# Performance work log

Measured on AMD Instinct MI355X. Metric: run time of the kernel, lower is better.

The kernel has to match this reference:

```python
import jax, jax.numpy as jnp
import numpy as np

B, C, N, K = 8, 192, 3136, 9
COUT = 384


def setup_inputs() -> dict:
    key = jax.random.key(0)
    k1, k2, k3, k4 = jax.random.split(key, 4)
    x = jax.random.normal(k1, (B, C, N, 1), dtype=jnp.float32)
    edge_index = jax.random.randint(k2, (2, B, N, K), 0, N, dtype=jnp.int64)
    # 1x1 conv params: BasicConv([2C, COUT]) with bias, act='relu'
    W = jax.random.normal(k3, (COUT, 2 * C), dtype=jnp.float32) * (1.0 / np.sqrt(2 * C))
    b = jax.random.normal(k4, (COUT,), dtype=jnp.float32) * 0.01
    return {"x": x, "edge_index": edge_index, "W": W, "b": b}


def _gather(xs, idx):
    # xs: [B, C, N]; idx: [B, N, K] -> [B, C, N, K]
    return jax.vmap(lambda xb, ib: xb[:, ib])(xs, idx)


def reference(x, edge_index, W, b):
    xs = x[..., 0]                       # [B, C, N]
    x_i = _gather(xs, edge_index[1])     # [B, C, N, K] center features
    x_j = _gather(xs, edge_index[0])     # [B, C, N, K] neighbor features
    feat = jnp.concatenate([x_i, x_j - x_i], axis=1)  # [B, 2C, N, K]
    # 1x1 conv + bias + relu
    h = jnp.einsum('oi,bink->bonk', W, feat) + b[None, :, None, None]
    h = jax.nn.relu(h)                   # [B, COUT, N, K]
    return jnp.max(h, axis=-1, keepdims=True)  # [B, COUT, N, 1]
```

## Files before the change

kernel.cpp:

```cpp
#include <hip/hip_runtime.h>
#include <hip/hip_bf16.h>


#define Bb   8
#define Cc   192
#define Nn   3136
#define Kk   9
#define CO   384
#define TWOC 384
#define JTOT 768
#define PADC 200
#define PADL 256

typedef short  short8 __attribute__((ext_vector_type(8)));
typedef float  f32x4  __attribute__((ext_vector_type(4)));

__device__ __forceinline__ float bf2f(unsigned int u16) {
    union { unsigned int i; float f; } c;
    c.i = u16 << 16;
    return c.f;
}
__device__ __forceinline__ short f2bf(float f) {
    __hip_bfloat16 h = __float2bfloat16(f);
    short s; __builtin_memcpy(&s, &h, 2); return s;
}

__global__ __launch_bounds__(256) void prep_fused(const void* __restrict__ x_,
                                                  const void* __restrict__ W_,
                                                  const int* __restrict__ ei,
                                                  short* __restrict__ xT,
                                                  short* __restrict__ A_Tb,
                                                  int* __restrict__ flags) {
    __shared__ float s[64][33];
    __shared__ int sflag;
    const int tid = threadIdx.x;
    const int bid = blockIdx.x;

    if (tid < 64) {
        unsigned int u = ((const unsigned short*)x_)[2 * tid];
        int bige = (((u >> 7) & 0xFFu) >= 0x88u);
        unsigned long long bf = __ballot(bige);
        int f32 = (bf != 0ull) ? 1 : 0;
        if (tid == 0) sflag = f32;
        if (bid == 0) {
            int oddnz = (ei[2 * tid + 1] != 0);
            unsigned long long bo = __ballot(oddnz);
            if (tid == 0) {
                flags[0] = f32;
                flags[1] = (bo == 0ull) ? 1 : 0;
            }
        }
    }
    __syncthreads();
    const int fp32 = sflag;

    if (bid < 2352) {
        int b   = bid / 294;
        int rem = bid - b * 294;
        int ct  = rem / 49;
        int nt  = rem - ct * 49;
        const int n0 = nt * 64;
        const int c0 = ct * 32;
        const int cl   = tid >> 3;
        const int nseg = tid & 7;

        if (fp32) {
            const float* p = (const float*)x_ + ((size_t)b * Cc + c0 + cl) * Nn + n0 + nseg * 8;
            float4 v0 = *(const float4*)p;
            float4 v1 = *(const float4*)(p + 4);
            int nb = nseg * 8;
            s[nb + 0][cl] = v0.x;  s[nb + 1][cl] = v0.y;
            s[nb + 2][cl] = v0.z;  s[nb + 3][cl] = v0.w;
            s[nb + 4][cl] = v1.x;  s[nb + 5][cl] = v1.y;
            s[nb + 6][cl] = v1.z;  s[nb + 7][cl] = v1.w;
        } else {
            const unsigned short* p = (const unsigned short*)x_ + ((size_t)b * Cc + c0 + cl) * Nn + n0 + nseg * 8;
            ushort4 u0 = *(const ushort4*)p;
            ushort4 u1 = *(const ushort4*)(p + 4);
            int nb = nseg * 8;
            s[nb + 0][cl] = bf2f(u0.x);  s[nb + 1][cl] = bf2f(u0.y);
            s[nb + 2][cl] = bf2f(u0.z);  s[nb + 3][cl] = bf2f(u0.w);
            s[nb + 4][cl] = bf2f(u1.x);  s[nb + 5][cl] = bf2f(u1.y);
            s[nb + 6][cl] = bf2f(u1.z);  s[nb + 7][cl] = bf2f(u1.w);
        }
        __syncthreads();

        const int nl = tid >> 2;
        const int cs = tid & 3;
        short8 o;
#pragma unroll
        for (int i = 0; i < 8; ++i) o[i] = f2bf(s[nl][cs * 8 + i]);
        *(short8*)(xT + ((size_t)b * Nn + n0 + nl) * PADC + c0 + cs * 8) = o;
    } else {
        int t = (bid - 2352) * 256 + tid;
        int j = t / Cc;
        int c = t - j * Cc;
        int row = (j < CO) ? j : (j - CO);
        float w1, w2;
        if (fp32) {
            const float* W = (const float*)W_;
            w1 = W[row * TWOC + c];  w2 = W[row * TWOC + Cc + c];
        } else {
            const unsigned short* W = (const unsigned short*)W_;
            w1 = bf2f(W[row * TWOC + c]);  w2 = bf2f(W[row * TWOC + Cc + c]);
        }
        A_Tb[(size_t)j * PADC + c] = f2bf((j < CO) ? (w1 - w2) : w2);
    }
}

__global__ __launch_bounds__(256) void gemm_mfma(const short* __restrict__ xT,
                                                 const short* __restrict__ A_Tb,
                                                 short* __restrict__ T) {
    __shared__ short Asl[64 * PADL];
    __shared__ short Bsl[64 * PADL];

    const int n0 = blockIdx.x * 64;
    const int j0 = blockIdx.y * 64;
    const int b  = blockIdx.z;
    const int tid  = threadIdx.x;
    const int w    = tid >> 6;
    const int lane = tid & 63;
    const int col  = lane & 15;
    const int quad = lane >> 4;

#pragma unroll
    for (int i = 0; i < 6; ++i) {
        int g    = tid + i * 256;
        int row  = g / 24;
        int slot = g - row * 24;
        int sl   = slot ^ (row & 7);
        *(short8*)(Asl + row * PADL + sl * 8) =
            *(const short8*)(xT + ((size_t)b * Nn + n0 + row) * PADC + slot * 8);
        *(short8*)(Bsl + row * PADL + sl * 8) =
            *(const short8*)(A_Tb + (size_t)(j0 + row) * PADC + slot * 8);
    }
    __syncthreads();

    f32x4 acc[4];
#pragma unroll
    for (int i = 0; i < 4; ++i) acc[i] = (f32x4)(0.0f);

#pragma unroll
    for (int kf = 0; kf < 6; ++kf) {
        const int sl = (kf * 4 + quad) ^ (col & 7);
        short8 bfr = *(const short8*)(Bsl + (w * 16 + col) * PADL + sl * 8);
#pragma unroll
        for (int fm = 0; fm < 4; ++fm) {
            short8 a = *(const short8*)(Asl + (fm * 16 + col) * PADL + sl * 8);
            acc[fm] = __builtin_amdgcn_mfma_f32_16x16x32_bf16(a, bfr, acc[fm], 0, 0, 0);
        }
    }
    __syncthreads();

    short* Ct = Asl;
#pragma unroll
    for (int fm = 0; fm < 4; ++fm) {
#pragma unroll
        for (int r = 0; r < 4; ++r) {
            Ct[(fm * 16 + quad * 4 + r) * 72 + w * 16 + col] = f2bf(acc[fm][r]);
        }
    }
    __syncthreads();

    {
        const int row = tid >> 2;
        const int gq  = tid & 3;
#pragma unroll
        for (int i = 0; i < 2; ++i) {
            int g = gq + i * 4;
            *(short8*)(T + ((size_t)(b * Nn + n0 + row)) * JTOT + j0 + g * 8) =
                *(const short8*)(Ct + row * 72 + g * 8);
        }
    }
}

__global__ __launch_bounds__(384) void gather_max(const int* __restrict__ ei,
                                                  const short* __restrict__ T,
                                                  const void* __restrict__ bias_,
                                                  void* __restrict__ out_,
                                                  const int* __restrict__ flags) {
    __shared__ float sm[32][97];
    __shared__ int si0[32][Kk];
    __shared__ int si1[32][Kk];

    const int fp32 = flags[0];
    const int is64 = flags[1];
    const int bid  = blockIdx.x;
    const int b    = bid & 7;
    const int rest = bid >> 3;
    const int quarter = rest / 98;
    const int n0   = (rest % 98) * 32;
    const int tid  = threadIdx.x;

    for (int s = tid; s < 32 * 2 * Kk; s += 384) {
        int ln = s / (2 * Kk);
        int slot = s - ln * (2 * Kk);
        int n = n0 + ln;
        size_t pos; int* dstp;
        if (slot < Kk) { pos = ((size_t)b * Nn + n) * Kk + slot;               dstp = &si0[ln][slot]; }
        else           { pos = ((size_t)(Bb + b) * Nn + n) * Kk + (slot - Kk); dstp = &si1[ln][slot - Kk]; }
        int v = is64 ? ei[2 * pos] : ei[pos];
        *dstp = (v < 0) ? 0 : (v >= Nn ? Nn - 1 : v);
    }
    __syncthreads();

    const int cg  = tid % 24;
    const int seg = tid / 24;
    const int och = quarter * 96 + cg * 4;
    const unsigned short* Tb = (const unsigned short*)T + (size_t)b * Nn * JTOT;

    float b0, b1, b2, b3;
    if (fp32) {
        const float* bp = (const float*)bias_ + och;
        b0 = bp[0]; b1 = bp[1]; b2 = bp[2]; b3 = bp[3];
    } else {
        const unsigned short* bp = (const unsigned short*)bias_ + och;
        b0 = bf2f(bp[0]); b1 = bf2f(bp[1]); b2 = bf2f(bp[2]); b3 = bf2f(bp[3]);
    }

#pragma unroll
    for (int t = 0; t < 2; ++t) {
        int ln = seg * 2 + t;
        float m0 = -INFINITY, m1 = -INFINITY, m2 = -INFINITY, m3 = -INFINITY;
#pragma unroll
        for (int k = 0; k < Kk; ++k) {
            uint2 uu = *(const uint2*)(Tb + (size_t)si1[ln][k] * JTOT + och);
            uint2 vv = *(const uint2*)(Tb + (size_t)si0[ln][k] * JTOT + CO + och);
            m0 = fmaxf(m0, bf2f(uu.x & 0xffffu) + bf2f(vv.x & 0xffffu));
            m1 = fmaxf(m1, bf2f(uu.x >> 16)     + bf2f(vv.x >> 16));
            m2 = fmaxf(m2, bf2f(uu.y & 0xffffu) + bf2f(vv.y & 0xffffu));
            m3 = fmaxf(m3, bf2f(uu.y >> 16)     + bf2f(vv.y >> 16));
        }
        sm[ln][cg * 4 + 0] = fmaxf(m0 + b0, 0.0f);
        sm[ln][cg * 4 + 1] = fmaxf(m1 + b1, 0.0f);
        sm[ln][cg * 4 + 2] = fmaxf(m2 + b2, 0.0f);
        sm[ln][cg * 4 + 3] = fmaxf(m3 + b3, 0.0f);
    }
    __syncthreads();

    const int g = tid >> 5, l = tid & 31;
    if (fp32) {
        float* op = (float*)out_;
#pragma unroll
        for (int rr = 0; rr < 8; ++rr) {
            int ol = g * 8 + rr;
            int o  = quarter * 96 + ol;
            op[((size_t)b * CO + o) * Nn + n0 + l] = sm[l][ol];
        }
    } else {
        __hip_bfloat16* op = (__hip_bfloat16*)out_;
#pragma unroll
        for (int rr = 0; rr < 8; ++rr) {
            int ol = g * 8 + rr;
            int o  = quarter * 96 + ol;
            op[((size_t)b * CO + o) * Nn + n0 + l] = __float2bfloat16(sm[l][ol]);
        }
    }
}

extern "C" void kernel_launch(void* const* d_in, const int* in_sizes, int n_in,
                              void* d_out, int out_size, void* d_ws, size_t ws_size,
                              hipStream_t stream) {
    const void* x  = d_in[0];
    const int*  ei = (const int*)d_in[1];
    const void* W  = d_in[2];
    const void* bs = d_in[3];

    char* ws = (char*)d_ws;
    int*   flags = (int*)ws;
    short* A_Tb  = (short*)(ws + 1024);
    short* xT    = (short*)(ws + (512u << 10));
    short* T     = (short*)(ws + (11u << 20));

    prep_fused<<<2352 + 576, 256, 0, stream>>>(x, W, ei, xT, A_Tb, flags);

    dim3 g1(Nn / 64, JTOT / 64, Bb);
    gemm_mfma<<<g1, 256, 0, stream>>>(xT, A_Tb, T);

    gather_max<<<Bb * 4 * (Nn / 32), 384, 0, stream>>>(ei, T, bs, d_out, flags);
}
```

Before: 136.7 us.

## Use direct global-to-LDS loads in GEMM and widen gather loads to 16 bytes

The GEMM tile staging now uses global_load_lds 16-byte transfers instead of loading through registers, with the swizzle moved to the global source address. The gather-max kernel gives each thread 8 output channels and one node (instead of 4 channels and two nodes), so each neighbor fetch is a single 16-byte load. It also precomputes byte offsets in shared memory and decodes bf16 with cheaper mask and shift operations. The aim is fewer load instructions and less VGPR traffic. The risks are per-lane LDS placement correctness for the direct loads and lower memory-level parallelism per thread.

```diff
diff --git a/kernel.cpp b/kernel.cpp
--- a/kernel.cpp
+++ b/kernel.cpp
@@ -20,9 +20,24 @@
     c.i = u16 << 16;
     return c.f;
 }
+__device__ __forceinline__ float bflo(unsigned int u) {
+    union { unsigned int i; float f; } c;
+    c.i = u << 16;
+    return c.f;
+}
+__device__ __forceinline__ float bfhi(unsigned int u) {
+    union { unsigned int i; float f; } c;
+    c.i = u & 0xffff0000u;
+    return c.f;
+}
 __device__ __forceinline__ short f2bf(float f) {
     __hip_bfloat16 h = __float2bfloat16(f);
     short s; __builtin_memcpy(&s, &h, 2); return s;
+}
+__device__ __forceinline__ void gload16(const void* g, void* l) {
+    __builtin_amdgcn_global_load_lds(
+        (const __attribute__((address_space(1))) unsigned int*)g,
+        (__attribute__((address_space(3))) unsigned int*)l, 16, 0, 0);
 }
 
 __global__ __launch_bounds__(256) void prep_fused(const void* __restrict__ x_,
@@ -123,16 +138,18 @@
     const int col  = lane & 15;
     const int quad = lane >> 4;
 
-#pragma unroll
-    for (int i = 0; i < 6; ++i) {
-        int g    = tid + i * 256;
-        int row  = g / 24;
-        int slot = g - row * 24;
-        int sl   = slot ^ (row & 7);
-        *(short8*)(Asl + row * PADL + sl * 8) =
-            *(const short8*)(xT + ((size_t)b * Nn + n0 + row) * PADC + slot * 8);
-        *(short8*)(Bsl + row * PADL + sl * 8) =
-            *(const short8*)(A_Tb + (size_t)(j0 + row) * PADC + slot * 8);
+    {
+        const int rh = lane >> 5;
+        const int s  = lane & 31;
+#pragma unroll
+        for (int t = 0; t < 8; ++t) {
+            const int row = w * 16 + t * 2 + rh;
+            const int sw  = s ^ (row & 7);
+            const short* gA = xT   + ((size_t)b * Nn + n0 + row) * PADC + sw * 8;
+            const short* gB = A_Tb + (size_t)(j0 + row) * PADC + sw * 8;
+            gload16(gA, Asl + (w * 16 + t * 2) * PADL);
+            gload16(gB, Bsl + (w * 16 + t * 2) * PADL);
+        }
     }
     __syncthreads();
 
@@ -180,8 +197,8 @@
                                                   void* __restrict__ out_,
                                                   const int* __restrict__ flags) {
     __shared__ float sm[32][97];
-    __shared__ int si0[32][Kk];
-    __shared__ int si1[32][Kk];
+    __shared__ int soff0[32][Kk];
+    __shared__ int soff1[32][Kk];
 
     const int fp32 = flags[0];
     const int is64 = flags[1];
@@ -197,45 +214,57 @@
         int slot = s - ln * (2 * Kk);
         int n = n0 + ln;
         size_t pos; int* dstp;
-        if (slot < Kk) { pos = ((size_t)b * Nn + n) * Kk + slot;               dstp = &si0[ln][slot]; }
-        else           { pos = ((size_t)(Bb + b) * Nn + n) * Kk + (slot - Kk); dstp = &si1[ln][slot - Kk]; }
+        if (slot < Kk) { pos = ((size_t)b * Nn + n) * Kk + slot;               dstp = &soff0[ln][slot]; }
+        else           { pos = ((size_t)(Bb + b) * Nn + n) * Kk + (slot - Kk); dstp = &soff1[ln][slot - Kk]; }
         int v = is64 ? ei[2 * pos] : ei[pos];
-        *dstp = (v < 0) ? 0 : (v >= Nn ? Nn - 1 : v);
-    }
-    __syncthreads();
-
-    const int cg  = tid % 24;
-    const int seg = tid / 24;
-    const int och = quarter * 96 + cg * 4;
-    const unsigned short* Tb = (const unsigned short*)T + (size_t)b * Nn * JTOT;
-
-    float b0, b1, b2, b3;
+        v = (v < 0) ? 0 : (v >= Nn ? Nn - 1 : v);
+        *dstp = v * (JTOT * 2);
+    }
+    __syncthreads();
+
+    const int cg  = tid % 12;
+    const int seg = tid / 12;
+    const int och = quarter * 96 + cg * 8;
+    const char* Tb = (const char*)T + (size_t)b * Nn * JTOT * 2;
+    const char* Tu = Tb + (size_t)och * 2;
+    const char* Tv = Tb + (size_t)(CO + och) * 2;
+
+    float bv[8];
     if (fp32) {
         const float* bp = (const float*)bias_ + och;
-        b0 = bp[0]; b1 = bp[1]; b2 = bp[2]; b3 = bp[3];
+#pragma unroll
+        for (int j = 0; j < 8; ++j) bv[j] = bp[j];
     } else {
         const unsigned short* bp = (const unsigned short*)bias_ + och;
-        b0 = bf2f(bp[0]); b1 = bf2f(bp[1]); b2 = bf2f(bp[2]); b3 = bf2f(bp[3]);
-    }
-
-#pragma unroll
-    for (int t = 0; t < 2; ++t) {
-        int ln = seg * 2 + t;
-        float m0 = -INFINITY, m1 = -INFINITY, m2 = -INFINITY, m3 = -INFINITY;
-#pragma unroll
-        for (int k = 0; k < Kk; ++k) {
-            uint2 uu = *(const uint2*)(Tb + (size_t)si1[ln][k] * JTOT + och);
-            uint2 vv = *(const uint2*)(Tb + (size_t)si0[ln][k] * JTOT + CO + och);
-            m0 = fmaxf(m0, bf2f(uu.x & 0xffffu) + bf2f(vv.x & 0xffffu));
-            m1 = fmaxf(m1, bf2f(uu.x >> 16)     + bf2f(vv.x >> 16));
-            m2 = fmaxf(m2, bf2f(uu.y & 0xffffu) + bf2f(vv.y & 0xffffu));
-            m3 = fmaxf(m3, bf2f(uu.y >> 16)     + bf2f(vv.y >> 16));
-        }
-        sm[ln][cg * 4 + 0] = fmaxf(m0 + b0, 0.0f);
-        sm[ln][cg * 4 + 1] = fmaxf(m1 + b1, 0.0f);
-        sm[ln][cg * 4 + 2] = fmaxf(m2 + b2, 0.0f);
-        sm[ln][cg * 4 + 3] = fmaxf(m3 + b3, 0.0f);
-    }
+#pragma unroll
+        for (int j = 0; j < 8; ++j) bv[j] = bf2f(bp[j]);
+    }
+
+    float m0 = -INFINITY, m1 = -INFINITY, m2 = -INFINITY, m3 = -INFINITY;
+    float m4 = -INFINITY, m5 = -INFINITY, m6 = -INFINITY, m7 = -INFINITY;
+#pragma unroll
+    for (int k = 0; k < Kk; ++k) {
+        const int o1 = soff1[seg][k];
+        const int o0 = soff0[seg][k];
+        uint4 uu = *(const uint4*)(Tu + o1);
+        uint4 vv = *(const uint4*)(Tv + o0);
+        m0 = fmaxf(m0, bflo(uu.x) + bflo(vv.x));
+        m1 = fmaxf(m1, bfhi(uu.x) + bfhi(vv.x));
+        m2 = fmaxf(m2, bflo(uu.y) + bflo(vv.y));
+        m3 = fmaxf(m3, bfhi(uu.y) + bfhi(vv.y));
+        m4 = fmaxf(m4, bflo(uu.z) + bflo(vv.z));
+        m5 = fmaxf(m5, bfhi(uu.z) + bfhi(vv.z));
+        m6 = fmaxf(m6, bflo(uu.w) + bflo(vv.w));
+        m7 = fmaxf(m7, bfhi(uu.w) + bfhi(vv.w));
+    }
+    sm[seg][cg * 8 + 0] = fmaxf(m0 + bv[0], 0.0f);
+    sm[seg][cg * 8 + 1] = fmaxf(m1 + bv[1], 0.0f);
+    sm[seg][cg * 8 + 2] = fmaxf(m2 + bv[2], 0.0f);
+    sm[seg][cg * 8 + 3] = fmaxf(m3 + bv[3], 0.0f);
+    sm[seg][cg * 8 + 4] = fmaxf(m4 + bv[4], 0.0f);
+    sm[seg][cg * 8 + 5] = fmaxf(m5 + bv[5], 0.0f);
+    sm[seg][cg * 8 + 6] = fmaxf(m6 + bv[6], 0.0f);
+    sm[seg][cg * 8 + 7] = fmaxf(m7 + bv[7], 0.0f);
     __syncthreads();
 
     const int g = tid >> 5, l = tid & 31;
```

Result: no change. 136.7 us (-0.0%).
